# Optimization experiments

Hardware: AMD Instinct MI355X
Metric: run time of the kernel (lower is better)

Reference implementation:

```python
import jax, jax.numpy as jnp
import numpy as np

B, S, D, H = 2, 2048, 1024, 16
HD = D // H


def setup_inputs() -> dict:
    key = jax.random.key(0)
    ks = jax.random.split(key, 5)
    x = jax.random.normal(ks[0], (B, S, D), dtype=jnp.float32)
    qk_w = jax.random.normal(ks[1], (D, 2 * D), dtype=jnp.float32) * 0.02
    qk_b = jnp.zeros((2 * D,), dtype=jnp.float32)
    v_w = jax.random.normal(ks[2], (D, D), dtype=jnp.float32) * 0.02
    cproj_w = jax.random.normal(ks[3], (D, D), dtype=jnp.float32) * 0.02
    resid_gain = jnp.ones((1, H, 1, 1), dtype=jnp.float32)
    skip_gain = jnp.ones((1, H, 1, 1), dtype=jnp.float32)
    centre_gain = jnp.ones((1, H, 1, 1), dtype=jnp.float32)
    return {"x": x, "qk_w": qk_w, "qk_b": qk_b, "v_w": v_w,
            "cproj_w": cproj_w, "resid_gain": resid_gain,
            "skip_gain": skip_gain, "centre_gain": centre_gain}


def reference(x, qk_w, qk_b, v_w, cproj_w, resid_gain, skip_gain, centre_gain):
    b, s, d = x.shape
    h, hd = H, d // H
    # fused QK projection (pconv with bias)
    qk = x @ qk_w + qk_b                      # [B,S,2D]
    q, k = jnp.split(qk, 2, axis=-1)
    v = x @ v_w                               # [B,S,D] (pconv, bias=0)
    # split heads -> [B,H,S,hd]
    q = q.reshape(b, s, h, hd).transpose(0, 2, 1, 3)
    k = k.reshape(b, s, h, hd).transpose(0, 2, 1, 3)
    v = v.reshape(b, s, h, hd).transpose(0, 2, 1, 3)
    # scaled QK^T with causal mask
    scores = jnp.einsum('bhqd,bhkd->bhqk', q, k) / jnp.sqrt(jnp.float32(hd))
    causal = jnp.tril(jnp.ones((s, s), dtype=bool))
    neg = jnp.finfo(scores.dtype).min
    scores = jnp.where(causal, scores, neg)
    attn = jax.nn.softmax(scores, axis=-1)    # [B,H,S,S]
    # shaped attention: per-head resid gain + skip (identity) - centred uniform causal
    row = jnp.arange(1, s + 1, dtype=jnp.float32)
    uniform = jnp.tril(jnp.ones((s, s), dtype=jnp.float32) / row[:, None])  # [S,S]
    eye = jnp.eye(s, dtype=jnp.float32)
    new_attn = (resid_gain * attn
                + skip_gain * eye[None, None]
                - centre_gain * uniform[None, None])
    out = jnp.einsum('bhqk,bhkd->bhqd', new_attn, v)  # [B,H,S,hd]
    out = out.transpose(0, 2, 1, 3).reshape(b, s, d)  # merge heads
    out = out @ cproj_w                                # c_proj (bias=0)
    return out
```

## Files before the change

### kernel.cpp

```cpp
#include <hip/hip_runtime.h>
#include <hip/hip_bf16.h>


typedef __hip_bfloat16 bf16;
typedef short s16x8 __attribute__((ext_vector_type(8)));
typedef short s16x4 __attribute__((ext_vector_type(4)));
typedef float f32x4 __attribute__((ext_vector_type(4)));

#define NB 2
#define NS 2048
#define ND 1024
#define NH 16
#define NHD 64
#define QSCALE 0.18033688011112042f
#define SW(r) (((r) & 7) << 4)

__device__ __forceinline__ float b2f(unsigned short u) {
  union { float f; unsigned int i; } c; c.i = ((unsigned int)u) << 16; return c.f;
}

__device__ __forceinline__ unsigned short f2bu(float f) {
  bf16 t = __float2bfloat16(f);
  unsigned short u;
  __builtin_memcpy(&u, &t, 2);
  return u;
}

__device__ __forceinline__ void gload_lds16(const void* g, void* l) {
  __builtin_amdgcn_global_load_lds((const __attribute__((address_space(1))) void*)g,
                                   (__attribute__((address_space(3))) void*)l, 16, 0, 0);
}

__global__ __launch_bounds__(256) void prologue(const float* __restrict__ x,
                                                const float* __restrict__ qk_w,
                                                const float* __restrict__ v_w,
                                                const float* __restrict__ cp_w,
                                                bf16* __restrict__ xb,
                                                bf16* __restrict__ qkwt,
                                                bf16* __restrict__ vwt,
                                                bf16* __restrict__ cpwt) {
  const int z = blockIdx.z;
  const int tx = threadIdx.x, ty = threadIdx.y;
  if (z == 0) {
    const int lb = (int)blockIdx.x + 64 * (int)blockIdx.y;
    const int base = lb * 2048 + (ty * 32 + tx) * 8;
    float4 v0 = *(const float4*)(x + base);
    float4 v1 = *(const float4*)(x + base + 4);
    ushort4 o0, o1;
    o0.x = f2bu(v0.x); o0.y = f2bu(v0.y); o0.z = f2bu(v0.z); o0.w = f2bu(v0.w);
    o1.x = f2bu(v1.x); o1.y = f2bu(v1.y); o1.z = f2bu(v1.z); o1.w = f2bu(v1.w);
    *(ushort4*)(xb + base) = o0;
    *(ushort4*)(xb + base + 4) = o1;
    return;
  }
  const int N = (z == 1) ? 2048 : 1024;
  if ((int)blockIdx.x * 32 >= N) return;
  const float* in = (z == 1) ? qk_w : (z == 2) ? v_w : cp_w;
  bf16* out = (z == 1) ? qkwt : (z == 2) ? vwt : cpwt;
  const int K = 1024;
  __shared__ float tile[32][33];
  int nt = blockIdx.x * 32, kt = blockIdx.y * 32;
#pragma unroll
  for (int j = 0; j < 32; j += 8)
    tile[ty + j][tx] = in[(size_t)(kt + ty + j) * N + nt + tx];
  __syncthreads();
#pragma unroll
  for (int j = 0; j < 32; j += 8)
    out[(size_t)(nt + ty + j) * K + kt + tx] = __float2bfloat16(tile[tx][ty + j]);
}

__global__ __launch_bounds__(256) void gemm_qkv(const bf16* __restrict__ A,
                                                const bf16* __restrict__ BtQK,
                                                const bf16* __restrict__ BtV,
                                                const float* __restrict__ bias,
                                                bf16* __restrict__ qo, bf16* __restrict__ ko,
                                                bf16* __restrict__ vo) {
  __shared__ alignas(16) bf16 As[128 * 64];
  __shared__ alignas(16) bf16 Bs[128 * 64];
  const int K = 1024;
  const int tid = threadIdx.x;
  const int wave = tid >> 6, lane = tid & 63;
  const int l15 = lane & 15, lg = lane >> 4;
  const int wr = wave >> 1, wc = wave & 1;
  const int brow = blockIdx.y * 128, bcol = blockIdx.x * 128;
  const bf16* Bsrc = (bcol < 2048) ? (BtQK + (size_t)bcol * K)
                                   : (BtV + (size_t)(bcol - 2048) * K);

  f32x4 acc[4][4] = {};
  const int sr = tid >> 3;
  const int sc = (tid & 7) * 8;
  char* AsB = (char*)As;
  char* BsB = (char*)Bs;

  for (int k0 = 0; k0 < K; k0 += 64) {
#pragma unroll
    for (int c = 0; c < 4; ++c) {
      gload_lds16(A + (size_t)(brow + c * 32 + sr) * K + k0 + sc, AsB + c * 4096 + tid * 16);
      gload_lds16(Bsrc + (size_t)(c * 32 + sr) * K + k0 + sc, BsB + c * 4096 + tid * 16);
    }
    __syncthreads();
#pragma unroll
    for (int kk = 0; kk < 2; ++kk) {
      s16x8 af[4], bfr[4];
#pragma unroll
      for (int mi = 0; mi < 4; ++mi)
        af[mi] = *(const s16x8*)(As + (wr * 64 + mi * 16 + l15) * 64 + kk * 32 + lg * 8);
#pragma unroll
      for (int ni = 0; ni < 4; ++ni)
        bfr[ni] = *(const s16x8*)(Bs + (wc * 64 + ni * 16 + l15) * 64 + kk * 32 + lg * 8);
#pragma unroll
      for (int mi = 0; mi < 4; ++mi)
#pragma unroll
        for (int ni = 0; ni < 4; ++ni)
          acc[mi][ni] = __builtin_amdgcn_mfma_f32_16x16x32_bf16(af[mi], bfr[ni], acc[mi][ni], 0, 0, 0);
    }
    __syncthreads();
  }

#pragma unroll
  for (int mi = 0; mi < 4; ++mi)
#pragma unroll
    for (int ni = 0; ni < 4; ++ni)
#pragma unroll
      for (int r = 0; r < 4; ++r) {
        int row = brow + wr * 64 + mi * 16 + lg * 4 + r;
        int col = bcol + wc * 64 + ni * 16 + l15;
        float v = acc[mi][ni][r];
        int b = row >> 11, s = row & 2047;
        int cc = col & 1023;
        int h = cc >> 6, e = cc & 63;
        if (col < 1024) {
          v = (v + bias[col]) * QSCALE;
          qo[((((size_t)b * NH + h) * NS) + s) * NHD + e] = __float2bfloat16(v);
        } else if (col < 2048) {
          v += bias[col];
          ko[((((size_t)b * NH + h) * NS) + s) * NHD + e] = __float2bfloat16(v);
        } else {
          vo[((((size_t)b * NH + h) * NHD) + e) * NS + s] = __float2bfloat16(v);
        }
      }
}

__global__ __launch_bounds__(256) void gemm_out(const bf16* __restrict__ A,
                                                const bf16* __restrict__ Bt,
                                                float* __restrict__ of) {
  __shared__ alignas(16) bf16 As[128 * 64];
  __shared__ alignas(16) bf16 Bs[64 * 64];
  const int K = 1024, N = 1024;
  const int tid = threadIdx.x;
  const int wave = tid >> 6, lane = tid & 63;
  const int l15 = lane & 15, lg = lane >> 4;
  const int brow = blockIdx.y * 128, bcol = blockIdx.x * 64;

  f32x4 acc[2][4] = {};
  const int sr = tid >> 3;
  const int sc = (tid & 7) * 8;
  char* AsB = (char*)As;
  char* BsB = (char*)Bs;

  for (int k0 = 0; k0 < K; k0 += 64) {
#pragma unroll
    for (int c = 0; c < 4; ++c)
      gload_lds16(A + (size_t)(brow + c * 32 + sr) * K + k0 + sc, AsB + c * 4096 + tid * 16);
#pragma unroll
    for (int c = 0; c < 2; ++c)
      gload_lds16(Bt + (size_t)(bcol + c * 32 + sr) * K + k0 + sc, BsB + c * 4096 + tid * 16);
    __syncthreads();
#pragma unroll
    for (int kk = 0; kk < 2; ++kk) {
      s16x8 af[2], bfr[4];
#pragma unroll
      for (int mi = 0; mi < 2; ++mi)
        af[mi] = *(const s16x8*)(As + (wave * 32 + mi * 16 + l15) * 64 + kk * 32 + lg * 8);
#pragma unroll
      for (int ni = 0; ni < 4; ++ni)
        bfr[ni] = *(const s16x8*)(Bs + (ni * 16 + l15) * 64 + kk * 32 + lg * 8);
#pragma unroll
      for (int mi = 0; mi < 2; ++mi)
#pragma unroll
        for (int ni = 0; ni < 4; ++ni)
          acc[mi][ni] = __builtin_amdgcn_mfma_f32_16x16x32_bf16(af[mi], bfr[ni], acc[mi][ni], 0, 0, 0);
    }
    __syncthreads();
  }

#pragma unroll
  for (int mi = 0; mi < 2; ++mi)
#pragma unroll
    for (int ni = 0; ni < 4; ++ni)
#pragma unroll
      for (int r = 0; r < 4; ++r) {
        int row = brow + wave * 32 + mi * 16 + lg * 4 + r;
        int col = bcol + ni * 16 + l15;
        of[(size_t)row * N + col] = acc[mi][ni][r];
      }
}

__global__ __launch_bounds__(512, 4) void attn_kernel(const bf16* __restrict__ qb,
                                                      const bf16* __restrict__ kb,
                                                      const bf16* __restrict__ vtb,
                                                      const float* __restrict__ rg,
                                                      const float* __restrict__ sg,
                                                      const float* __restrict__ cg,
                                                      bf16* __restrict__ out) {
  const int hb = blockIdx.x;
  const int h = hb & 15, b = hb >> 4;
  const int j = blockIdx.y;
  const int tid = threadIdx.x, wave = tid >> 6, lane = tid & 63;
  const int l15 = lane & 15, lg = lane >> 4;
  const int grp = wave >> 2, wv4 = wave & 3;
  const int qt = grp ? (31 - j) : j;
  const int ntm1 = 31 - j;

  __shared__ alignas(16) char Ks[2][64 * 128];
  __shared__ alignas(16) char Vs[2][64 * 128];
  __shared__ alignas(16) char Pl[8][2048];
  char* Plw = Pl[wave];
  const int swz = ((((l15 >> 3) ^ l15) & 7) << 4);

  const size_t hoff = ((size_t)b * NH + h) * NS * NHD;
  const bf16* K = kb + hoff;
  const bf16* VT = vtb + hoff;
  const float rgh = rg[h], sgh = sg[h], cgh = cg[h];

  const int qbase = qt * 64 + wv4 * 16;
  const int qloc = wv4 * 16 + l15;

  const bf16* Q = qb + hoff;
  s16x8 qa0 = *(const s16x8*)(Q + (size_t)(qbase + l15) * NHD + lg * 8);
  s16x8 qa1 = *(const s16x8*)(Q + (size_t)(qbase + l15) * NHD + 32 + lg * 8);

  const short ONE = 0x3F80;
  const s16x8 ones = {ONE, ONE, ONE, ONE, ONE, ONE, ONE, ONE};
  s16x8 pc0, pc1;
#pragma unroll
  for (int jj = 0; jj < 8; ++jj) {
    pc0[jj] = (lg * 8 + jj <= qloc) ? ONE : (short)0;
    pc1[jj] = (32 + lg * 8 + jj <= qloc) ? ONE : (short)0;
  }

  f32x4 acc_o[4] = {};
  f32x4 acc_c[4] = {};
  f32x4 acc_l = {};

  const int srow = tid >> 3;
  const int sce = (tid & 7) * 8;
  const int scb = (sce * 2) ^ SW(srow);

  s16x8 kra = *(const s16x8*)(K + (size_t)srow * NHD + sce);
  s16x8 vra = *(const s16x8*)(VT + (size_t)srow * NS + sce);

  for (int t = 0; t <= ntm1; ++t) {
    char* Kb = Ks[t & 1];
    char* Vb = Vs[t & 1];
    *(s16x8*)(Kb + srow * 128 + scb) = kra;
    *(s16x8*)(Vb + srow * 128 + scb) = vra;
    if (t < ntm1) {
      kra = *(const s16x8*)(K + ((size_t)(t + 1) * 64 + srow) * NHD + sce);
      vra = *(const s16x8*)(VT + (size_t)srow * NS + (t + 1) * 64 + sce);
    }
    __syncthreads();

    if (t > qt) continue;
    const bool diag = (t == qt);

    f32x4 sc[4] = {};
    __builtin_amdgcn_s_setprio(1);
#pragma unroll
    for (int c = 0; c < 4; ++c) {
      const int R = c * 16 + l15;
      s16x8 kf0 = *(const s16x8*)(Kb + R * 128 + ((lg * 16) ^ SW(R)));
      s16x8 kf1 = *(const s16x8*)(Kb + R * 128 + ((64 + lg * 16) ^ SW(R)));
      sc[c] = __builtin_amdgcn_mfma_f32_16x16x32_bf16(kf0, qa0, sc[c], 0, 0, 0);
      sc[c] = __builtin_amdgcn_mfma_f32_16x16x32_bf16(kf1, qa1, sc[c], 0, 0, 0);
    }
    __builtin_amdgcn_s_setprio(0);

    if (diag) {
#pragma unroll
      for (int c = 0; c < 4; ++c)
#pragma unroll
        for (int r = 0; r < 4; ++r)
          if (c * 16 + lg * 4 + r > qloc) sc[c][r] = -INFINITY;
    }

#pragma unroll
    for (int c = 0; c < 4; ++c) {
      s16x4 pk;
      pk[0] = (short)f2bu(exp2f(sc[c][0]));
      pk[1] = (short)f2bu(exp2f(sc[c][1]));
      pk[2] = (short)f2bu(exp2f(sc[c][2]));
      pk[3] = (short)f2bu(exp2f(sc[c][3]));
      *(s16x4*)(Plw + l15 * 128 + ((c * 32 + lg * 8) ^ swz)) = pk;
    }
    s16x8 pa0 = *(const s16x8*)(Plw + l15 * 128 + ((lg * 16) ^ swz));
    s16x8 pa1 = *(const s16x8*)(Plw + l15 * 128 + ((64 + lg * 16) ^ swz));

    const s16x8 qc0 = diag ? pc0 : ones;
    const s16x8 qc1 = diag ? pc1 : ones;

    __builtin_amdgcn_s_setprio(1);
    acc_l = __builtin_amdgcn_mfma_f32_16x16x32_bf16(pa0, ones, acc_l, 0, 0, 0);
    acc_l = __builtin_amdgcn_mfma_f32_16x16x32_bf16(pa1, ones, acc_l, 0, 0, 0);
#pragma unroll
    for (int sub = 0; sub < 4; ++sub) {
      const int Rv = sub * 16 + l15;
      s16x8 vf0 = *(const s16x8*)(Vb + Rv * 128 + ((lg * 16) ^ SW(Rv)));
      s16x8 vf1 = *(const s16x8*)(Vb + Rv * 128 + ((64 + lg * 16) ^ SW(Rv)));
      acc_o[sub] = __builtin_amdgcn_mfma_f32_16x16x32_bf16(pa0, vf0, acc_o[sub], 0, 0, 0);
      acc_o[sub] = __builtin_amdgcn_mfma_f32_16x16x32_bf16(pa1, vf1, acc_o[sub], 0, 0, 0);
      acc_c[sub] = __builtin_amdgcn_mfma_f32_16x16x32_bf16(qc0, vf0, acc_c[sub], 0, 0, 0);
      acc_c[sub] = __builtin_amdgcn_mfma_f32_16x16x32_bf16(qc1, vf1, acc_c[sub], 0, 0, 0);
    }
    __builtin_amdgcn_s_setprio(0);

    if (diag) {
      float linv[4];
#pragma unroll
      for (int r = 0; r < 4; ++r) linv[r] = 1.0f / acc_l[r];
#pragma unroll
      for (int sub = 0; sub < 4; ++sub) {
        const int d = sub * 16 + l15;
        const int cb = wv4 * 32 + lg * 8;
        s16x4 vr4 = *(const s16x4*)(Vb + d * 128 + (cb ^ SW(d)));
        unsigned short vbits[4];
        __builtin_memcpy(vbits, &vr4, 8);
#pragma unroll
        for (int r = 0; r < 4; ++r) {
          int q = qbase + lg * 4 + r;
          float val = rgh * acc_o[sub][r] * linv[r] + sgh * b2f(vbits[r]) -
                      cgh * acc_c[sub][r] / (float)(q + 1);
          out[((size_t)b * NS + q) * ND + h * NHD + d] = __float2bfloat16(val);
        }
      }
    }
  }
}

extern "C" void kernel_launch(void* const* d_in, const int* in_sizes, int n_in,
                              void* d_out, int out_size, void* d_ws, size_t ws_size,
                              hipStream_t stream) {
  const float* x = (const float*)d_in[0];
  const float* qk_w = (const float*)d_in[1];
  const float* qk_b = (const float*)d_in[2];
  const float* v_w = (const float*)d_in[3];
  const float* cproj_w = (const float*)d_in[4];
  const float* rg = (const float*)d_in[5];
  const float* sg = (const float*)d_in[6];
  const float* cg = (const float*)d_in[7];
  float* out = (float*)d_out;

  char* p = (char*)d_ws;
  bf16* xb = (bf16*)p;   p += (size_t)4096 * 1024 * 2;
  bf16* qkwt = (bf16*)p; p += (size_t)2048 * 1024 * 2;
  bf16* vwt = (bf16*)p;  p += (size_t)1024 * 1024 * 2;
  bf16* cpwt = (bf16*)p; p += (size_t)1024 * 1024 * 2;
  bf16* qbuf = (bf16*)p; p += (size_t)NB * NH * NS * NHD * 2;
  bf16* kbuf = (bf16*)p; p += (size_t)NB * NH * NS * NHD * 2;
  bf16* vtbuf = (bf16*)p; p += (size_t)NB * NH * NS * NHD * 2;
  bf16* aout = (bf16*)p; p += (size_t)4096 * 1024 * 2;

  prologue<<<dim3(64, 32, 4), dim3(32, 8), 0, stream>>>(x, qk_w, v_w, cproj_w,
                                                        xb, qkwt, vwt, cpwt);
  gemm_qkv<<<dim3(24, 32), 256, 0, stream>>>(xb, qkwt, vwt, qk_b, qbuf, kbuf, vtbuf);
  attn_kernel<<<dim3(32, 16), 512, 0, stream>>>(qbuf, kbuf, vtbuf, rg, sg, cg, aout);
  gemm_out<<<dim3(16, 32), 256, 0, stream>>>(aout, cpwt, out);
}
```

Before: 119.9 us.

## Split GEMM LDS tiles into k-halves and remap blocks for XCD locality

```diff
diff --git a/kernel.cpp b/kernel.cpp
--- a/kernel.cpp
+++ b/kernel.cpp
@@ -75,28 +75,32 @@
                                                 const float* __restrict__ bias,
                                                 bf16* __restrict__ qo, bf16* __restrict__ ko,
                                                 bf16* __restrict__ vo) {
-  __shared__ alignas(16) bf16 As[128 * 64];
-  __shared__ alignas(16) bf16 Bs[128 * 64];
+  __shared__ alignas(16) bf16 As[2][128 * 32];
+  __shared__ alignas(16) bf16 Bs[2][128 * 32];
   const int K = 1024;
   const int tid = threadIdx.x;
   const int wave = tid >> 6, lane = tid & 63;
   const int l15 = lane & 15, lg = lane >> 4;
   const int wr = wave >> 1, wc = wave & 1;
-  const int brow = blockIdx.y * 128, bcol = blockIdx.x * 128;
+  const int bid = (int)blockIdx.x + (int)blockIdx.y * 24;
+  const int sbid = (bid & 7) * 96 + (bid >> 3);
+  const int brow = (sbid / 24) * 128, bcol = (sbid % 24) * 128;
   const bf16* Bsrc = (bcol < 2048) ? (BtQK + (size_t)bcol * K)
                                    : (BtV + (size_t)(bcol - 2048) * K);
 
   f32x4 acc[4][4] = {};
-  const int sr = tid >> 3;
-  const int sc = (tid & 7) * 8;
+  const int srw = tid >> 2;
+  const int scl = (tid & 3) * 8;
   char* AsB = (char*)As;
   char* BsB = (char*)Bs;
 
   for (int k0 = 0; k0 < K; k0 += 64) {
 #pragma unroll
-    for (int c = 0; c < 4; ++c) {
-      gload_lds16(A + (size_t)(brow + c * 32 + sr) * K + k0 + sc, AsB + c * 4096 + tid * 16);
-      gload_lds16(Bsrc + (size_t)(c * 32 + sr) * K + k0 + sc, BsB + c * 4096 + tid * 16);
+    for (int q = 0; q < 4; ++q) {
+      const int grow = (q & 1) * 64 + srw;
+      const int gk = (q >> 1) * 32 + scl;
+      gload_lds16(A + (size_t)(brow + grow) * K + k0 + gk, AsB + q * 4096 + tid * 16);
+      gload_lds16(Bsrc + (size_t)grow * K + k0 + gk, BsB + q * 4096 + tid * 16);
     }
     __syncthreads();
 #pragma unroll
@@ -104,10 +108,10 @@
       s16x8 af[4], bfr[4];
 #pragma unroll
       for (int mi = 0; mi < 4; ++mi)
-        af[mi] = *(const s16x8*)(As + (wr * 64 + mi * 16 + l15) * 64 + kk * 32 + lg * 8);
+        af[mi] = *(const s16x8*)(As[kk] + (wr * 64 + mi * 16 + l15) * 32 + lg * 8);
 #pragma unroll
       for (int ni = 0; ni < 4; ++ni)
-        bfr[ni] = *(const s16x8*)(Bs + (wc * 64 + ni * 16 + l15) * 64 + kk * 32 + lg * 8);
+        bfr[ni] = *(const s16x8*)(Bs[kk] + (wc * 64 + ni * 16 + l15) * 32 + lg * 8);
 #pragma unroll
       for (int mi = 0; mi < 4; ++mi)
 #pragma unroll
@@ -144,37 +148,43 @@
 __global__ __launch_bounds__(256) void gemm_out(const bf16* __restrict__ A,
                                                 const bf16* __restrict__ Bt,
                                                 float* __restrict__ of) {
-  __shared__ alignas(16) bf16 As[128 * 64];
-  __shared__ alignas(16) bf16 Bs[64 * 64];
+  __shared__ alignas(16) bf16 As[2][128 * 32];
+  __shared__ alignas(16) bf16 Bs[2][64 * 32];
   const int K = 1024, N = 1024;
   const int tid = threadIdx.x;
   const int wave = tid >> 6, lane = tid & 63;
   const int l15 = lane & 15, lg = lane >> 4;
-  const int brow = blockIdx.y * 128, bcol = blockIdx.x * 64;
+  const int bid = (int)blockIdx.x + (int)blockIdx.y * 16;
+  const int sbid = (bid & 7) * 64 + (bid >> 3);
+  const int brow = (sbid / 16) * 128, bcol = (sbid % 16) * 64;
 
   f32x4 acc[2][4] = {};
-  const int sr = tid >> 3;
-  const int sc = (tid & 7) * 8;
+  const int srw = tid >> 2;
+  const int scl = (tid & 3) * 8;
   char* AsB = (char*)As;
   char* BsB = (char*)Bs;
 
   for (int k0 = 0; k0 < K; k0 += 64) {
 #pragma unroll
-    for (int c = 0; c < 4; ++c)
-      gload_lds16(A + (size_t)(brow + c * 32 + sr) * K + k0 + sc, AsB + c * 4096 + tid * 16);
-#pragma unroll
-    for (int c = 0; c < 2; ++c)
-      gload_lds16(Bt + (size_t)(bcol + c * 32 + sr) * K + k0 + sc, BsB + c * 4096 + tid * 16);
+    for (int q = 0; q < 4; ++q) {
+      const int grow = (q & 1) * 64 + srw;
+      const int gk = (q >> 1) * 32 + scl;
+      gload_lds16(A + (size_t)(brow + grow) * K + k0 + gk, AsB + q * 4096 + tid * 16);
+    }
+#pragma unroll
+    for (int q = 0; q < 2; ++q) {
+      gload_lds16(Bt + (size_t)(bcol + srw) * K + k0 + q * 32 + scl, BsB + q * 4096 + tid * 16);
+    }
     __syncthreads();
 #pragma unroll
     for (int kk = 0; kk < 2; ++kk) {
       s16x8 af[2], bfr[4];
 #pragma unroll
       for (int mi = 0; mi < 2; ++mi)
-        af[mi] = *(const s16x8*)(As + (wave * 32 + mi * 16 + l15) * 64 + kk * 32 + lg * 8);
+        af[mi] = *(const s16x8*)(As[kk] + (wave * 32 + mi * 16 + l15) * 32 + lg * 8);
 #pragma unroll
       for (int ni = 0; ni < 4; ++ni)
-        bfr[ni] = *(const s16x8*)(Bs + (ni * 16 + l15) * 64 + kk * 32 + lg * 8);
+        bfr[ni] = *(const s16x8*)(Bs[kk] + (ni * 16 + l15) * 32 + lg * 8);
 #pragma unroll
       for (int mi = 0; mi < 2; ++mi)
 #pragma unroll
```

New measurement: 133.2 us. 11.1% more time.
